# Kernel optimization log

Hardware: AMD Instinct MI355X
Metric: run time of the kernel (lower is better)

Reference implementation:

```python
import jax, jax.numpy as jnp
import numpy as np
from math import ceil

B, T, FEAT, F1, ACTION_DIM, ATOMS = 128, 128, 256, 512, 6, 32


def _make_masks(f1, action_dim, atoms):
    # Faithful numpy replication of ActorMultiEnv_v2.create_weigth_mask
    sz = action_dim * atoms
    aux1, aux2 = sz, f1
    dvs = [0]
    w = np.zeros([f1, sz], np.float32)
    we = np.zeros([f1, f1], np.float32)
    for i in range(sz):
        dv = aux2 / aux1
        v = ceil(dv) if dv - int(dv) > 0.5 else int(dv)
        s = int(np.sum(dvs))
        w[s:s + v, i] = 1.0 / v
        we[s:s + v, s:s + v] = 1.0
        dvs.append(v)
        aux1 -= 1
        aux2 -= v
    sizes = np.array([3, 5, 7, 9, 11, 15, 19, 25, 35])
    m = int(sizes[np.argmin(np.abs(max(dvs[1:]) - sizes))])
    return w, we, m, int(ceil(f1 / m))


def setup_inputs() -> dict:
    key = jax.random.key(0)
    ks = jax.random.split(key, 16)

    def he(k, shape):
        return jax.random.normal(k, shape, jnp.float32) * np.float32(np.sqrt(2.0 / shape[0]))

    w_np, we_np, m, sz_mini = _make_masks(F1, ACTION_DIM, ATOMS)
    return {
        "features": jax.random.normal(ks[0], (B, T, FEAT), jnp.float32),
        "W_hat1": he(ks[1], (FEAT, F1)),
        "M_hat1": he(ks[2], (FEAT, F1)),
        "G1": he(ks[3], (FEAT, F1)),
        "W_hat2": he(ks[4], (F1, F1)),
        "M_hat2": he(ks[5], (F1, F1)),
        "G2": he(ks[6], (F1, F1)),
        "W1e": he(ks[7], (2 * F1, F1)),
        "b1e": jnp.zeros((F1,), jnp.float32),
        "W2e": he(ks[8], (F1, F1)),
        "b2e": jnp.zeros((F1,), jnp.float32),
        "W3": he(ks[9], (F1, F1)),
        "b3": jnp.zeros((F1,), jnp.float32),
        "kn": he(ks[10], (m, m)),
        "w": jnp.asarray(w_np),
        "we": jnp.asarray(we_np),
        "sz_mini": sz_mini,
        "action_dim": ACTION_DIM,
        "atoms": ATOMS,
    }


def _nalu_pair(x1, x2, W_hat, M_hat, G):
    # NALU transform with two stacked output branches (additive, gated-nalu)
    W = jnp.tanh(W_hat) * jax.nn.sigmoid(M_hat)
    a = x1 @ W
    m = jnp.exp(jnp.clip(jnp.log(jnp.abs(x2) + 1e-7) @ W, -20.0, 20.0))
    g = jax.nn.sigmoid(x1 @ G)
    return jax.nn.gelu(a), jax.nn.gelu(g * a + (1.0 - g) * m)


def reference(features, W_hat1, M_hat1, G1, W_hat2, M_hat2, G2,
              W1e, b1e, W2e, b2e, W3, b3, kn, w, we,
              sz_mini, action_dim, atoms):
    # fc1 / fc2 (nalu_transform): two stacked branches on axis 1
    h11, h12 = _nalu_pair(features, features, W_hat1, M_hat1, G1)   # [B,T,f1] each
    ha, ht = _nalu_pair(h11, h12, W_hat2, M_hat2, G2)
    h = jnp.concatenate([ha, ht], axis=-1)                           # [B,T,2*f1]

    f1 = we.shape[0]
    # block-diagonal tiling of the per-env mini-kernel, masked by 'we'
    Keff = jnp.kron(jnp.eye(sz_mini, dtype=kn.dtype), kn)[:f1, :f1] * we  # [f1,f1]

    xa1 = jax.nn.gelu((h @ W1e + b1e) @ Keff)    # fc1e: dense -> block-masked mini-kernel matmul
    xa2 = jax.nn.gelu((xa1 @ W2e + b2e) @ Keff)  # fc2e
    v = xa2 @ (W3 * we) + b3                     # fc3: masked dense
    o = (xa1 @ w).reshape(xa1.shape[0], xa1.shape[1], action_dim, atoms)
    return o, v
```

## Files before the change

### kernel.cpp

```cpp
#include <hip/hip_runtime.h>
#include <hip/hip_bf16.h>
#include <hip/hip_fp16.h>

#define NROWS 16384
#define FEATD 256
#define F1D   512
#define SZD   192

typedef unsigned short u16;
typedef float    f32x4  __attribute__((ext_vector_type(4)));
typedef short    bf16x8 __attribute__((ext_vector_type(8)));
typedef _Float16 f16x8  __attribute__((ext_vector_type(8)));
typedef unsigned short u16x8 __attribute__((ext_vector_type(8)));

#define LO_SCALE 2048.0f
#define LO_INV   (1.0f / 2048.0f)

__device__ __forceinline__ float sigmoid_f(float x) { return 1.0f / (1.0f + expf(-x)); }

__device__ __forceinline__ float gelu_f(float x) {
    float x3 = x * x * x;
    float inner = 0.7978845608028654f * (x + 0.044715f * x3);
    return 0.5f * x * (1.0f + tanhf(inner));
}

__device__ __forceinline__ u16 f2bf(float f) {
    unsigned u = __float_as_uint(f);
    u = (u + 0x7FFFu + ((u >> 16) & 1u)) >> 16;
    return (u16)u;
}
__device__ __forceinline__ float bf2f(u16 h) { return __uint_as_float(((unsigned)h) << 16); }

__device__ __forceinline__ void split8(float4 a, float4 b, u16x8& hi, u16x8& lo) {
    float v[8] = {a.x, a.y, a.z, a.w, b.x, b.y, b.z, b.w};
    #pragma unroll
    for (int i = 0; i < 8; ++i) {
        u16 h = f2bf(v[i]);
        hi[i] = h;
        lo[i] = f2bf(v[i] - bf2f(h));
    }
}

__device__ __forceinline__ u16 f2h_u(float f)  { return __half_as_ushort(__float2half(f)); }
__device__ __forceinline__ float h2f_u(u16 u)  { return __half2float(__ushort_as_half(u)); }

__device__ __forceinline__ void split8hs(float4 a, float4 b, u16x8& hi, u16x8& lo) {
    float v[8] = {a.x, a.y, a.z, a.w, b.x, b.y, b.z, b.w};
    #pragma unroll
    for (int i = 0; i < 8; ++i) {
        u16 h = f2h_u(v[i]);
        hi[i] = h;
        lo[i] = f2h_u((v[i] - h2f_u(h)) * LO_SCALE);
    }
}

__device__ __forceinline__ int lofs(int row, int chunk) {
    return row * 32 + ((chunk ^ ((row >> 1) & 3)) << 3);
}

__global__ void wprep_f16_kernel(const float* __restrict__ src, const float* __restrict__ src2,
                                 u16* __restrict__ dhi, u16* __restrict__ dlo, int Kd, int Nd)
{
    int idx = blockIdx.x * blockDim.x + threadIdx.x;
    if (idx >= Kd * Nd) return;
    int n = idx / Kd, k = idx - n * Kd;
    float v = src[(size_t)k * Nd + n];
    if (src2) v = tanhf(v) * sigmoid_f(src2[(size_t)k * Nd + n]);
    u16 h = f2h_u(v);
    dhi[idx] = h;
    dlo[idx] = f2h_u((v - h2f_u(h)) * LO_SCALE);
}

__global__ void wprep2_kernel(const float* __restrict__ src,
                              u16* __restrict__ dhi, u16* __restrict__ dlo, int Kd, int Nd)
{
    int idx = blockIdx.x * blockDim.x + threadIdx.x;
    if (idx >= Kd * Nd) return;
    int n = idx / Kd, k = idx - n * Kd;
    float v = src[(size_t)k * Nd + n];
    u16 h = f2bf(v);
    dhi[idx] = h;
    dlo[idx] = f2bf(v - bf2f(h));
}

__global__ __launch_bounds__(512)
void prep2_kernel(const float* __restrict__ kn, const float* __restrict__ we,
                  const float* __restrict__ W3,
                  float* __restrict__ Kb, float* __restrict__ W3b, int m)
{
    int j = threadIdx.x;
    if (j >= F1D) return;
    int jb = (j / m) * m;
    int jm = j - jb;
    for (int t = 0; t < 4; ++t) {
        int i = jb + t;
        float v = 0.0f;
        if (t < m && i < F1D)
            v = kn[t * m + jm] * we[(size_t)i * F1D + j];
        Kb[t * F1D + j] = v;
    }
    for (int d = 0; d < 15; ++d) {
        int i = j - 7 + d;
        float v = 0.0f;
        if (i >= 0 && i < F1D)
            v = W3[(size_t)i * F1D + j] * we[(size_t)i * F1D + j];
        W3b[d * F1D + j] = v;
    }
}

__global__ void colrange_wband_kernel(const float* __restrict__ w, int* __restrict__ cs,
                                      float* __restrict__ wb)
{
    int c = blockIdx.x * blockDim.x + threadIdx.x;
    if (c >= SZD) return;
    int s = 0, e = -1;
    for (int r = 0; r < F1D; ++r) {
        if (w[(size_t)r * SZD + c] != 0.0f) { if (e < 0) s = r; e = r; }
    }
    cs[c] = s;
    for (int t = 0; t < 4; ++t)
        wb[t * SZD + c] = (s + t <= e) ? w[(size_t)(s + t) * SZD + c] : 0.0f;
}

template<int K, bool LOGX2, bool WRITE_LOG>
__global__ __launch_bounds__(256)
void nalu_mfma_kernel(const float* __restrict__ x1, const float* __restrict__ x2,
                      const u16* __restrict__ Wh, const u16* __restrict__ Wl,
                      const u16* __restrict__ Gh, const u16* __restrict__ Gl,
                      float* __restrict__ out1, float* __restrict__ out2, int ld_out)
{
    __shared__ u16 A1h[64 * 32], A1l[64 * 32];
    __shared__ u16 A2h[64 * 32], A2l[64 * 32];
    __shared__ u16 BWh[64 * 32], BWl[64 * 32];
    __shared__ u16 BGh[64 * 32], BGl[64 * 32];

    const int t = threadIdx.x;
    const int lane = t & 63;
    const int wv = t >> 6;
    const int wr = wv >> 1, wc = wv & 1;
    const int lr = lane & 15, lk = lane >> 4;
    const int row0 = blockIdx.y * 64;
    const int col0 = blockIdx.x * 64;
    const int sr = t >> 2;
    const int kc = t & 3;

    f32x4 aA[2][2], aAx[2][2], aM[2][2], aMx[2][2], aG[2][2], aGx[2][2];
    #pragma unroll
    for (int i = 0; i < 2; ++i)
        #pragma unroll
        for (int j = 0; j < 2; ++j) {
            aA[i][j] = 0; aAx[i][j] = 0;
            aM[i][j] = 0; aMx[i][j] = 0;
            aG[i][j] = 0; aGx[i][j] = 0;
        }

    for (int k0 = 0; k0 < K; k0 += 32) {
        const float* px1 = x1 + (size_t)(row0 + sr) * K + k0 + kc * 8;
        float4 f0 = *(const float4*)px1;
        float4 f1 = *(const float4*)(px1 + 4);
        u16x8 v1h, v1l;
        split8hs(f0, f1, v1h, v1l);
        float4 e0, e1;
        if (LOGX2) {
            e0.x = logf(fabsf(f0.x) + 1e-7f); e0.y = logf(fabsf(f0.y) + 1e-7f);
            e0.z = logf(fabsf(f0.z) + 1e-7f); e0.w = logf(fabsf(f0.w) + 1e-7f);
            e1.x = logf(fabsf(f1.x) + 1e-7f); e1.y = logf(fabsf(f1.y) + 1e-7f);
            e1.z = logf(fabsf(f1.z) + 1e-7f); e1.w = logf(fabsf(f1.w) + 1e-7f);
        } else {
            const float* px2 = x2 + (size_t)(row0 + sr) * K + k0 + kc * 8;
            e0 = *(const float4*)px2;
            e1 = *(const float4*)(px2 + 4);
        }
        u16x8 v2h, v2l;
        split8hs(e0, e1, v2h, v2l);
        u16x8 vwh = *(const u16x8*)(Wh + (size_t)(col0 + sr) * K + k0 + kc * 8);
        u16x8 vwl = *(const u16x8*)(Wl + (size_t)(col0 + sr) * K + k0 + kc * 8);
        u16x8 vgh = *(const u16x8*)(Gh + (size_t)(col0 + sr) * K + k0 + kc * 8);
        u16x8 vgl = *(const u16x8*)(Gl + (size_t)(col0 + sr) * K + k0 + kc * 8);

        __syncthreads();
        {
            int o = lofs(sr, kc);
            *(u16x8*)&A1h[o] = v1h;  *(u16x8*)&A1l[o] = v1l;
            *(u16x8*)&A2h[o] = v2h;  *(u16x8*)&A2l[o] = v2l;
            *(u16x8*)&BWh[o] = vwh;  *(u16x8*)&BWl[o] = vwl;
            *(u16x8*)&BGh[o] = vgh;  *(u16x8*)&BGl[o] = vgl;
        }
        __syncthreads();

        #pragma unroll
        for (int fc = 0; fc < 2; ++fc) {
            const int bo = lofs(wc * 32 + fc * 16 + lr, lk);
            f16x8 bwh = *(f16x8*)&BWh[bo];
            f16x8 bwl = *(f16x8*)&BWl[bo];
            f16x8 bgh = *(f16x8*)&BGh[bo];
            f16x8 bgl = *(f16x8*)&BGl[bo];
            #pragma unroll
            for (int fr = 0; fr < 2; ++fr) {
                const int ao = lofs(wr * 32 + fr * 16 + lr, lk);
                f16x8 a1h = *(f16x8*)&A1h[ao];
                f16x8 a1l = *(f16x8*)&A1l[ao];
                f16x8 a2h = *(f16x8*)&A2h[ao];
                f16x8 a2l = *(f16x8*)&A2l[ao];
                aA [fr][fc] = __builtin_amdgcn_mfma_f32_16x16x32_f16(a1h, bwh, aA [fr][fc], 0, 0, 0);
                aAx[fr][fc] = __builtin_amdgcn_mfma_f32_16x16x32_f16(a1h, bwl, aAx[fr][fc], 0, 0, 0);
                aAx[fr][fc] = __builtin_amdgcn_mfma_f32_16x16x32_f16(a1l, bwh, aAx[fr][fc], 0, 0, 0);
                aM [fr][fc] = __builtin_amdgcn_mfma_f32_16x16x32_f16(a2h, bwh, aM [fr][fc], 0, 0, 0);
                aMx[fr][fc] = __builtin_amdgcn_mfma_f32_16x16x32_f16(a2h, bwl, aMx[fr][fc], 0, 0, 0);
                aMx[fr][fc] = __builtin_amdgcn_mfma_f32_16x16x32_f16(a2l, bwh, aMx[fr][fc], 0, 0, 0);
                aG [fr][fc] = __builtin_amdgcn_mfma_f32_16x16x32_f16(a1h, bgh, aG [fr][fc], 0, 0, 0);
                aGx[fr][fc] = __builtin_amdgcn_mfma_f32_16x16x32_f16(a1h, bgl, aGx[fr][fc], 0, 0, 0);
                aGx[fr][fc] = __builtin_amdgcn_mfma_f32_16x16x32_f16(a1l, bgh, aGx[fr][fc], 0, 0, 0);
            }
        }
    }

    #pragma unroll
    for (int fr = 0; fr < 2; ++fr)
        #pragma unroll
        for (int fc = 0; fc < 2; ++fc) {
            int colg = col0 + wc * 32 + fc * 16 + lr;
            int rowb = row0 + wr * 32 + fr * 16 + lk * 4;
            #pragma unroll
            for (int i = 0; i < 4; ++i) {
                float a  = aA[fr][fc][i] + aAx[fr][fc][i] * LO_INV;
                float mm = aM[fr][fc][i] + aMx[fr][fc][i] * LO_INV;
                float g  = aG[fr][fc][i] + aGx[fr][fc][i] * LO_INV;
                float m_ = expf(fminf(fmaxf(mm, -20.0f), 20.0f));
                float gs = sigmoid_f(g);
                float h11v = gelu_f(a);
                float h12v = gelu_f(gs * a + (1.0f - gs) * m_);
                out1[(size_t)(rowb + i) * ld_out + colg] = h11v;
                out2[(size_t)(rowb + i) * ld_out + colg] =
                    WRITE_LOG ? logf(fabsf(h12v) + 1e-7f) : h12v;
            }
        }
}

template<int K>
__global__ __launch_bounds__(256)
void gemm_mfma_kernel(const float* __restrict__ A,
                      const u16* __restrict__ Bh, const u16* __restrict__ Bl,
                      const float* __restrict__ bias, float* __restrict__ out)
{
    __shared__ u16 Ah[128 * 32], Al[128 * 32];
    __shared__ u16 Bsh[64 * 32], Bsl[64 * 32];

    const int t = threadIdx.x;
    const int lane = t & 63;
    const int wv = t >> 6;
    const int wr = wv >> 1, wc = wv & 1;
    const int lr = lane & 15, lk = lane >> 4;
    const int row0 = blockIdx.y * 128;
    const int col0 = blockIdx.x * 64;
    const int sr = t >> 2;
    const int kc = t & 3;

    f32x4 acc[4][2];
    #pragma unroll
    for (int i = 0; i < 4; ++i)
        #pragma unroll
        for (int j = 0; j < 2; ++j) acc[i][j] = 0;

    for (int k0 = 0; k0 < K; k0 += 32) {
        u16x8 vah[2], val[2];
        #pragma unroll
        for (int p = 0; p < 2; ++p) {
            int r = p * 64 + sr;
            const float* pa = A + (size_t)(row0 + r) * K + k0 + kc * 8;
            float4 f0 = *(const float4*)pa;
            float4 f1 = *(const float4*)(pa + 4);
            split8(f0, f1, vah[p], val[p]);
        }
        u16x8 vbh = *(const u16x8*)(Bh + (size_t)(col0 + sr) * K + k0 + kc * 8);
        u16x8 vbl = *(const u16x8*)(Bl + (size_t)(col0 + sr) * K + k0 + kc * 8);

        __syncthreads();
        #pragma unroll
        for (int p = 0; p < 2; ++p) {
            int o = lofs(p * 64 + sr, kc);
            *(u16x8*)&Ah[o] = vah[p];
            *(u16x8*)&Al[o] = val[p];
        }
        {
            int o = lofs(sr, kc);
            *(u16x8*)&Bsh[o] = vbh;
            *(u16x8*)&Bsl[o] = vbl;
        }
        __syncthreads();

        #pragma unroll
        for (int fc = 0; fc < 2; ++fc) {
            const int bo = lofs(wc * 32 + fc * 16 + lr, lk);
            bf16x8 bh = *(bf16x8*)&Bsh[bo];
            bf16x8 bl = *(bf16x8*)&Bsl[bo];
            #pragma unroll
            for (int fr = 0; fr < 4; ++fr) {
                const int ao = lofs(wr * 64 + fr * 16 + lr, lk);
                bf16x8 ah = *(bf16x8*)&Ah[ao];
                bf16x8 al = *(bf16x8*)&Al[ao];
                f32x4 a = acc[fr][fc];
                a = __builtin_amdgcn_mfma_f32_16x16x32_bf16(ah, bh, a, 0, 0, 0);
                a = __builtin_amdgcn_mfma_f32_16x16x32_bf16(ah, bl, a, 0, 0, 0);
                a = __builtin_amdgcn_mfma_f32_16x16x32_bf16(al, bh, a, 0, 0, 0);
                acc[fr][fc] = a;
            }
        }
    }

    #pragma unroll
    for (int fr = 0; fr < 4; ++fr)
        #pragma unroll
        for (int fc = 0; fc < 2; ++fc) {
            int colg = col0 + wc * 32 + fc * 16 + lr;
            int rowb = row0 + wr * 64 + fr * 16 + lk * 4;
            float bv = bias[colg];
            #pragma unroll
            for (int i = 0; i < 4; ++i)
                out[(size_t)(rowb + i) * F1D + colg] = acc[fr][fc][i] + bv;
        }
}

template<int ROWS>
__global__ __launch_bounds__(256)
void kxo_kernel(const float* __restrict__ pre1, const float* __restrict__ Kb,
                const float* __restrict__ wb, const int* __restrict__ cs,
                float* __restrict__ xa1, float* __restrict__ o_out, int m)
{
    __shared__ float sKb[4][F1D];
    __shared__ float swb[4][SZD];
    __shared__ int   scs[SZD];
    __shared__ float spre[2][F1D];
    __shared__ float sxa[2][F1D];

    const int t = threadIdx.x;
    for (int i = t; i < 4 * F1D; i += 256) sKb[i >> 9][i & 511] = Kb[i];
    for (int i = t; i < 4 * SZD; i += 256) swb[i / SZD][i % SZD] = wb[i];
    if (t < SZD) scs[t] = cs[t];

    const int row_base = blockIdx.x * ROWS;
    const int rr = t >> 7;
    const int jc = t & 127;

    for (int ch = 0; ch < ROWS; ch += 2) {
        const int r0 = row_base + ch;
        __syncthreads();
        ((float4*)&spre[0][0])[t] = *(const float4*)(pre1 + (size_t)r0 * F1D + t * 4);
        __syncthreads();

        #pragma unroll
        for (int kk = 0; kk < 4; ++kk) {
            int j  = jc + (kk << 7);
            int jb = (j / m) * m;
            float s = 0.0f;
            for (int tt = 0; tt < 4; ++tt) {
                int i2 = jb + tt; if (i2 > F1D - 1) i2 = F1D - 1;
                s = fmaf(spre[rr][i2], sKb[tt][j], s);
            }
            float g = gelu_f(s);
            sxa[rr][j] = g;
            xa1[(size_t)(r0 + rr) * F1D + j] = g;
        }
        __syncthreads();

        for (int pos = t; pos < 2 * SZD; pos += 256) {
            int rr2 = pos / SZD, c = pos - rr2 * SZD;
            int s0 = scs[c];
            float s = 0.0f;
            #pragma unroll
            for (int tt = 0; tt < 4; ++tt) {
                int i2 = s0 + tt; if (i2 > F1D - 1) i2 = F1D - 1;
                s = fmaf(sxa[rr2][i2], swb[tt][c], s);
            }
            o_out[(size_t)(r0 + rr2) * SZD + c] = s;
        }
    }
}

template<int ROWS>
__global__ __launch_bounds__(256)
void kv_kernel(const float* __restrict__ pre2, const float* __restrict__ Kb,
               const float* __restrict__ W3b, const float* __restrict__ b3,
               float* __restrict__ v_out, int m)
{
    __shared__ float sW3[15][F1D];
    __shared__ float sKb[4][F1D];
    __shared__ float sb3[F1D];
    __shared__ float spre[2][F1D];
    __shared__ float sxa[2][F1D];

    const int t = threadIdx.x;
    for (int i = t; i < 15 * F1D; i += 256) sW3[i >> 9][i & 511] = W3b[i];
    for (int i = t; i < 4 * F1D; i += 256)  sKb[i >> 9][i & 511] = Kb[i];
    for (int i = t; i < F1D; i += 256)      sb3[i] = b3[i];

    const int row_base = blockIdx.x * ROWS;
    const int rr = t >> 7;
    const int jc = t & 127;

    for (int ch = 0; ch < ROWS; ch += 2) {
        const int r0 = row_base + ch;
        __syncthreads();
        ((float4*)&spre[0][0])[t] = *(const float4*)(pre2 + (size_t)r0 * F1D + t * 4);
        __syncthreads();

        #pragma unroll
        for (int kk = 0; kk < 4; ++kk) {
            int j  = jc + (kk << 7);
            int jb = (j / m) * m;
            float s = 0.0f;
            for (int tt = 0; tt < 4; ++tt) {
                int i2 = jb + tt; if (i2 > F1D - 1) i2 = F1D - 1;
                s = fmaf(spre[rr][i2], sKb[tt][j], s);
            }
            sxa[rr][j] = gelu_f(s);
        }
        __syncthreads();

        #pragma unroll
        for (int kk = 0; kk < 4; ++kk) {
            int j = jc + (kk << 7);
            float s = sb3[j];
            #pragma unroll
            for (int d = 0; d < 15; ++d) {
                int i2 = j - 7 + d;
                if (i2 < 0) i2 = 0; if (i2 > F1D - 1) i2 = F1D - 1;
                s = fmaf(sxa[rr][i2], sW3[d][j], s);
            }
            v_out[(size_t)(r0 + rr) * F1D + j] = s;
        }
    }
}

extern "C" void kernel_launch(void* const* d_in, const int* in_sizes, int n_in,
                              void* d_out, int out_size, void* d_ws, size_t ws_size,
                              hipStream_t stream)
{
    const float* features = (const float*)d_in[0];
    const float* Wh1 = (const float*)d_in[1];
    const float* Mh1 = (const float*)d_in[2];
    const float* G1  = (const float*)d_in[3];
    const float* Wh2 = (const float*)d_in[4];
    const float* Mh2 = (const float*)d_in[5];
    const float* G2  = (const float*)d_in[6];
    const float* W1e = (const float*)d_in[7];
    const float* b1e = (const float*)d_in[8];
    const float* W2e = (const float*)d_in[9];
    const float* b2e = (const float*)d_in[10];
    const float* W3  = (const float*)d_in[11];
    const float* b3  = (const float*)d_in[12];
    const float* kn  = (const float*)d_in[13];
    const float* w   = (const float*)d_in[14];
    const float* we  = (const float*)d_in[15];

    int m = 1;
    { int s = in_sizes[13]; while (m * m < s) ++m; }

    char* base = (char*)d_ws;
    size_t off = 0;
    auto alloc = [&](size_t bytes) { void* p = base + off; off += (bytes + 255) & ~255ull; return p; };
    u16*   W1h  = (u16*)alloc((size_t)F1D * FEATD * 2);
    u16*   W1l  = (u16*)alloc((size_t)F1D * FEATD * 2);
    u16*   G1h  = (u16*)alloc((size_t)F1D * FEATD * 2);
    u16*   G1l  = (u16*)alloc((size_t)F1D * FEATD * 2);
    u16*   W2h  = (u16*)alloc((size_t)F1D * F1D * 2);
    u16*   W2l  = (u16*)alloc((size_t)F1D * F1D * 2);
    u16*   G2h  = (u16*)alloc((size_t)F1D * F1D * 2);
    u16*   G2l  = (u16*)alloc((size_t)F1D * F1D * 2);
    u16*   W1eh = (u16*)alloc((size_t)F1D * 2 * F1D * 2);
    u16*   W1el = (u16*)alloc((size_t)F1D * 2 * F1D * 2);
    u16*   W2eh = (u16*)alloc((size_t)F1D * F1D * 2);
    u16*   W2el = (u16*)alloc((size_t)F1D * F1D * 2);
    float* Kb   = (float*)alloc(4 * F1D * 4);
    float* W3b  = (float*)alloc(15 * F1D * 4);
    float* wb   = (float*)alloc(4 * SZD * 4);
    int*   cs   = (int*)alloc(SZD * 4);
    float* h11  = (float*)alloc((size_t)NROWS * F1D * 4);
    float* lh12 = (float*)alloc((size_t)NROWS * F1D * 4);
    float* hb   = (float*)alloc((size_t)NROWS * 2 * F1D * 4);

    float* o_out = (float*)d_out;
    float* v_out = (float*)d_out + (size_t)NROWS * SZD;
    float* xa1   = v_out;

    wprep_f16_kernel<<<(F1D * FEATD + 255) / 256, 256, 0, stream>>>(Wh1, Mh1, W1h, W1l, FEATD, F1D);
    wprep_f16_kernel<<<(F1D * FEATD + 255) / 256, 256, 0, stream>>>(G1, nullptr, G1h, G1l, FEATD, F1D);
    wprep_f16_kernel<<<(F1D * F1D + 255) / 256, 256, 0, stream>>>(Wh2, Mh2, W2h, W2l, F1D, F1D);
    wprep_f16_kernel<<<(F1D * F1D + 255) / 256, 256, 0, stream>>>(G2, nullptr, G2h, G2l, F1D, F1D);
    wprep2_kernel<<<(F1D * 2 * F1D + 255) / 256, 256, 0, stream>>>(W1e, W1eh, W1el, 2 * F1D, F1D);
    wprep2_kernel<<<(F1D * F1D + 255) / 256, 256, 0, stream>>>(W2e, W2eh, W2el, F1D, F1D);
    prep2_kernel<<<1, 512, 0, stream>>>(kn, we, W3, Kb, W3b, m);
    colrange_wband_kernel<<<1, 256, 0, stream>>>(w, cs, wb);

    dim3 gN(F1D / 64, NROWS / 64);
    dim3 gG(F1D / 64, NROWS / 128);

    nalu_mfma_kernel<FEATD, true, true><<<gN, 256, 0, stream>>>(
        features, features, W1h, W1l, G1h, G1l, h11, lh12, F1D);
    nalu_mfma_kernel<F1D, false, false><<<gN, 256, 0, stream>>>(
        h11, lh12, W2h, W2l, G2h, G2l, hb, hb + F1D, 2 * F1D);

    float* pre1 = h11;
    gemm_mfma_kernel<2 * F1D><<<gG, 256, 0, stream>>>(hb, W1eh, W1el, b1e, pre1);

    kxo_kernel<8><<<NROWS / 8, 256, 0, stream>>>(pre1, Kb, wb, cs, xa1, o_out, m);

    float* pre2 = lh12;
    gemm_mfma_kernel<F1D><<<gG, 256, 0, stream>>>(xa1, W2eh, W2el, b2e, pre2);

    kv_kernel<8><<<NROWS / 8, 256, 0, stream>>>(pre2, Kb, W3b, b3, v_out, m);
}
```

Before: 568.1 us.

## Store intermediates as pre-split hi/lo half pairs and swizzle tiles across XCDs

```diff
diff --git a/kernel.cpp b/kernel.cpp
--- a/kernel.cpp
+++ b/kernel.cpp
@@ -30,16 +30,6 @@
     return (u16)u;
 }
 __device__ __forceinline__ float bf2f(u16 h) { return __uint_as_float(((unsigned)h) << 16); }
-
-__device__ __forceinline__ void split8(float4 a, float4 b, u16x8& hi, u16x8& lo) {
-    float v[8] = {a.x, a.y, a.z, a.w, b.x, b.y, b.z, b.w};
-    #pragma unroll
-    for (int i = 0; i < 8; ++i) {
-        u16 h = f2bf(v[i]);
-        hi[i] = h;
-        lo[i] = f2bf(v[i] - bf2f(h));
-    }
-}
 
 __device__ __forceinline__ u16 f2h_u(float f)  { return __half_as_ushort(__float2half(f)); }
 __device__ __forceinline__ float h2f_u(u16 u)  { return __half2float(__ushort_as_half(u)); }
@@ -56,6 +46,15 @@
 
 __device__ __forceinline__ int lofs(int row, int chunk) {
     return row * 32 + ((chunk ^ ((row >> 1) & 3)) << 3);
+}
+
+__device__ __forceinline__ void xcd_tile(int TM, int& row0, int& col0) {
+    int b   = blockIdx.x + gridDim.x * blockIdx.y;
+    int nwg = gridDim.x * gridDim.y;
+    int q   = nwg >> 3;
+    int swz = (b & 7) * q + (b >> 3);
+    col0 = (swz & 7) * 64;
+    row0 = (swz >> 3) * TM;
 }
 
 __global__ void wprep_f16_kernel(const float* __restrict__ src, const float* __restrict__ src2,
@@ -122,12 +121,13 @@
         wb[t * SZD + c] = (s + t <= e) ? w[(size_t)(s + t) * SZD + c] : 0.0f;
 }
 
-template<int K, bool LOGX2, bool WRITE_LOG>
+template<int K>
 __global__ __launch_bounds__(256)
-void nalu_mfma_kernel(const float* __restrict__ x1, const float* __restrict__ x2,
-                      const u16* __restrict__ Wh, const u16* __restrict__ Wl,
-                      const u16* __restrict__ Gh, const u16* __restrict__ Gl,
-                      float* __restrict__ out1, float* __restrict__ out2, int ld_out)
+void nalu_l1_kernel(const float* __restrict__ x1,
+                    const u16* __restrict__ Wh, const u16* __restrict__ Wl,
+                    const u16* __restrict__ Gh, const u16* __restrict__ Gl,
+                    u16* __restrict__ o1h, u16* __restrict__ o1l,
+                    u16* __restrict__ o2h, u16* __restrict__ o2l)
 {
     __shared__ u16 A1h[64 * 32], A1l[64 * 32];
     __shared__ u16 A2h[64 * 32], A2l[64 * 32];
@@ -139,8 +139,8 @@
     const int wv = t >> 6;
     const int wr = wv >> 1, wc = wv & 1;
     const int lr = lane & 15, lk = lane >> 4;
-    const int row0 = blockIdx.y * 64;
-    const int col0 = blockIdx.x * 64;
+    int row0, col0;
+    xcd_tile(64, row0, col0);
     const int sr = t >> 2;
     const int kc = t & 3;
 
@@ -161,16 +161,10 @@
         u16x8 v1h, v1l;
         split8hs(f0, f1, v1h, v1l);
         float4 e0, e1;
-        if (LOGX2) {
-            e0.x = logf(fabsf(f0.x) + 1e-7f); e0.y = logf(fabsf(f0.y) + 1e-7f);
-            e0.z = logf(fabsf(f0.z) + 1e-7f); e0.w = logf(fabsf(f0.w) + 1e-7f);
-            e1.x = logf(fabsf(f1.x) + 1e-7f); e1.y = logf(fabsf(f1.y) + 1e-7f);
-            e1.z = logf(fabsf(f1.z) + 1e-7f); e1.w = logf(fabsf(f1.w) + 1e-7f);
-        } else {
-            const float* px2 = x2 + (size_t)(row0 + sr) * K + k0 + kc * 8;
-            e0 = *(const float4*)px2;
-            e1 = *(const float4*)(px2 + 4);
-        }
+        e0.x = logf(fabsf(f0.x) + 1e-7f); e0.y = logf(fabsf(f0.y) + 1e-7f);
+        e0.z = logf(fabsf(f0.z) + 1e-7f); e0.w = logf(fabsf(f0.w) + 1e-7f);
+        e1.x = logf(fabsf(f1.x) + 1e-7f); e1.y = logf(fabsf(f1.y) + 1e-7f);
+        e1.z = logf(fabsf(f1.z) + 1e-7f); e1.w = logf(fabsf(f1.w) + 1e-7f);
         u16x8 v2h, v2l;
         split8hs(e0, e1, v2h, v2l);
         u16x8 vwh = *(const u16x8*)(Wh + (size_t)(col0 + sr) * K + k0 + kc * 8);
@@ -230,29 +224,142 @@
                 float gs = sigmoid_f(g);
                 float h11v = gelu_f(a);
                 float h12v = gelu_f(gs * a + (1.0f - gs) * m_);
-                out1[(size_t)(rowb + i) * ld_out + colg] = h11v;
-                out2[(size_t)(rowb + i) * ld_out + colg] =
-                    WRITE_LOG ? logf(fabsf(h12v) + 1e-7f) : h12v;
+                float lgv  = logf(fabsf(h12v) + 1e-7f);
+                size_t oi = (size_t)(rowb + i) * F1D + colg;
+                u16 hh = f2h_u(h11v);
+                o1h[oi] = hh;
+                o1l[oi] = f2h_u((h11v - h2f_u(hh)) * LO_SCALE);
+                u16 lh = f2h_u(lgv);
+                o2h[oi] = lh;
+                o2l[oi] = f2h_u((lgv - h2f_u(lh)) * LO_SCALE);
             }
         }
 }
 
 template<int K>
 __global__ __launch_bounds__(256)
-void gemm_mfma_kernel(const float* __restrict__ A,
-                      const u16* __restrict__ Bh, const u16* __restrict__ Bl,
-                      const float* __restrict__ bias, float* __restrict__ out)
-{
-    __shared__ u16 Ah[128 * 32], Al[128 * 32];
-    __shared__ u16 Bsh[64 * 32], Bsl[64 * 32];
+void nalu_l2_kernel(const u16* __restrict__ x1h, const u16* __restrict__ x1l,
+                    const u16* __restrict__ x2h, const u16* __restrict__ x2l,
+                    const u16* __restrict__ Wh, const u16* __restrict__ Wl,
+                    const u16* __restrict__ Gh, const u16* __restrict__ Gl,
+                    u16* __restrict__ ohh, u16* __restrict__ ohl)
+{
+    __shared__ u16 A1h[64 * 32], A1l[64 * 32];
+    __shared__ u16 A2h[64 * 32], A2l[64 * 32];
+    __shared__ u16 BWh[64 * 32], BWl[64 * 32];
+    __shared__ u16 BGh[64 * 32], BGl[64 * 32];
 
     const int t = threadIdx.x;
     const int lane = t & 63;
     const int wv = t >> 6;
     const int wr = wv >> 1, wc = wv & 1;
     const int lr = lane & 15, lk = lane >> 4;
-    const int row0 = blockIdx.y * 128;
-    const int col0 = blockIdx.x * 64;
+    int row0, col0;
+    xcd_tile(64, row0, col0);
+    const int sr = t >> 2;
+    const int kc = t & 3;
+
+    f32x4 aA[2][2], aAx[2][2], aM[2][2], aMx[2][2], aG[2][2], aGx[2][2];
+    #pragma unroll
+    for (int i = 0; i < 2; ++i)
+        #pragma unroll
+        for (int j = 0; j < 2; ++j) {
+            aA[i][j] = 0; aAx[i][j] = 0;
+            aM[i][j] = 0; aMx[i][j] = 0;
+            aG[i][j] = 0; aGx[i][j] = 0;
+        }
+
+    for (int k0 = 0; k0 < K; k0 += 32) {
+        const size_t arow = (size_t)(row0 + sr) * K + k0 + kc * 8;
+        const size_t brow = (size_t)(col0 + sr) * K + k0 + kc * 8;
+        u16x8 v1h = *(const u16x8*)(x1h + arow);
+        u16x8 v1l = *(const u16x8*)(x1l + arow);
+        u16x8 v2h = *(const u16x8*)(x2h + arow);
+        u16x8 v2l = *(const u16x8*)(x2l + arow);
+        u16x8 vwh = *(const u16x8*)(Wh + brow);
+        u16x8 vwl = *(const u16x8*)(Wl + brow);
+        u16x8 vgh = *(const u16x8*)(Gh + brow);
+        u16x8 vgl = *(const u16x8*)(Gl + brow);
+
+        __syncthreads();
+        {
+            int o = lofs(sr, kc);
+            *(u16x8*)&A1h[o] = v1h;  *(u16x8*)&A1l[o] = v1l;
+            *(u16x8*)&A2h[o] = v2h;  *(u16x8*)&A2l[o] = v2l;
+            *(u16x8*)&BWh[o] = vwh;  *(u16x8*)&BWl[o] = vwl;
+            *(u16x8*)&BGh[o] = vgh;  *(u16x8*)&BGl[o] = vgl;
+        }
+        __syncthreads();
+
+        #pragma unroll
+        for (int fc = 0; fc < 2; ++fc) {
+            const int bo = lofs(wc * 32 + fc * 16 + lr, lk);
+            f16x8 bwh = *(f16x8*)&BWh[bo];
+            f16x8 bwl = *(f16x8*)&BWl[bo];
+            f16x8 bgh = *(f16x8*)&BGh[bo];
+            f16x8 bgl = *(f16x8*)&BGl[bo];
+            #pragma unroll
+            for (int fr = 0; fr < 2; ++fr) {
+                const int ao = lofs(wr * 32 + fr * 16 + lr, lk);
+                f16x8 a1h = *(f16x8*)&A1h[ao];
+                f16x8 a1l = *(f16x8*)&A1l[ao];
+                f16x8 a2h = *(f16x8*)&A2h[ao];
+                f16x8 a2l = *(f16x8*)&A2l[ao];
+                aA [fr][fc] = __builtin_amdgcn_mfma_f32_16x16x32_f16(a1h, bwh, aA [fr][fc], 0, 0, 0);
+                aAx[fr][fc] = __builtin_amdgcn_mfma_f32_16x16x32_f16(a1h, bwl, aAx[fr][fc], 0, 0, 0);
+                aAx[fr][fc] = __builtin_amdgcn_mfma_f32_16x16x32_f16(a1l, bwh, aAx[fr][fc], 0, 0, 0);
+                aM [fr][fc] = __builtin_amdgcn_mfma_f32_16x16x32_f16(a2h, bwh, aM [fr][fc], 0, 0, 0);
+                aMx[fr][fc] = __builtin_amdgcn_mfma_f32_16x16x32_f16(a2h, bwl, aMx[fr][fc], 0, 0, 0);
+                aMx[fr][fc] = __builtin_amdgcn_mfma_f32_16x16x32_f16(a2l, bwh, aMx[fr][fc], 0, 0, 0);
+                aG [fr][fc] = __builtin_amdgcn_mfma_f32_16x16x32_f16(a1h, bgh, aG [fr][fc], 0, 0, 0);
+                aGx[fr][fc] = __builtin_amdgcn_mfma_f32_16x16x32_f16(a1h, bgl, aGx[fr][fc], 0, 0, 0);
+                aGx[fr][fc] = __builtin_amdgcn_mfma_f32_16x16x32_f16(a1l, bgh, aGx[fr][fc], 0, 0, 0);
+            }
+        }
+    }
+
+    #pragma unroll
+    for (int fr = 0; fr < 2; ++fr)
+        #pragma unroll
+        for (int fc = 0; fc < 2; ++fc) {
+            int colg = col0 + wc * 32 + fc * 16 + lr;
+            int rowb = row0 + wr * 32 + fr * 16 + lk * 4;
+            #pragma unroll
+            for (int i = 0; i < 4; ++i) {
+                float a  = aA[fr][fc][i] + aAx[fr][fc][i] * LO_INV;
+                float mm = aM[fr][fc][i] + aMx[fr][fc][i] * LO_INV;
+                float g  = aG[fr][fc][i] + aGx[fr][fc][i] * LO_INV;
+                float m_ = expf(fminf(fmaxf(mm, -20.0f), 20.0f));
+                float gs = sigmoid_f(g);
+                float hav = gelu_f(a);
+                float htv = gelu_f(gs * a + (1.0f - gs) * m_);
+                size_t base = (size_t)(rowb + i) * (2 * F1D) + colg;
+                u16 ah = f2bf(hav);
+                ohh[base] = ah;
+                ohl[base] = f2bf(hav - bf2f(ah));
+                u16 th = f2bf(htv);
+                ohh[base + F1D] = th;
+                ohl[base + F1D] = f2bf(htv - bf2f(th));
+            }
+        }
+}
+
+template<int K>
+__global__ __launch_bounds__(256)
+void gemm_mfma_kernel(const u16* __restrict__ Ahp, const u16* __restrict__ Alp,
+                      const u16* __restrict__ Bh, const u16* __restrict__ Bl,
+                      const float* __restrict__ bias, float* __restrict__ out)
+{
+    __shared__ u16 Ah[128 * 32], Al[128 * 32];
+    __shared__ u16 Bsh[64 * 32], Bsl[64 * 32];
+
+    const int t = threadIdx.x;
+    const int lane = t & 63;
+    const int wv = t >> 6;
+    const int wr = wv >> 1, wc = wv & 1;
+    const int lr = lane & 15, lk = lane >> 4;
+    int row0, col0;
+    xcd_tile(128, row0, col0);
     const int sr = t >> 2;
     const int kc = t & 3;
 
@@ -266,14 +373,13 @@
         u16x8 vah[2], val[2];
         #pragma unroll
         for (int p = 0; p < 2; ++p) {
-            int r = p * 64 + sr;
-            const float* pa = A + (size_t)(row0 + r) * K + k0 + kc * 8;
-            float4 f0 = *(const float4*)pa;
-            float4 f1 = *(const float4*)(pa + 4);
-            split8(f0, f1, vah[p], val[p]);
-        }
-        u16x8 vbh = *(const u16x8*)(Bh + (size_t)(col0 + sr) * K + k0 + kc * 8);
-        u16x8 vbl = *(const u16x8*)(Bl + (size_t)(col0 + sr) * K + k0 + kc * 8);
+            const size_t arow = (size_t)(row0 + p * 64 + sr) * K + k0 + kc * 8;
+            vah[p] = *(const u16x8*)(Ahp + arow);
+            val[p] = *(const u16x8*)(Alp + arow);
+        }
+        const size_t brow = (size_t)(col0 + sr) * K + k0 + kc * 8;
+        u16x8 vbh = *(const u16x8*)(Bh + brow);
+        u16x8 vbl = *(const u16x8*)(Bl + brow);
 
         __syncthreads();
         #pragma unroll
@@ -325,7 +431,8 @@
 __global__ __launch_bounds__(256)
 void kxo_kernel(const float* __restrict__ pre1, const float* __restrict__ Kb,
                 const float* __restrict__ wb, const int* __restrict__ cs,
-                float* __restrict__ xa1, float* __restrict__ o_out, int m)
+                u16* __restrict__ xa1h, u16* __restrict__ xa1l,
+                float* __restrict__ o_out, int m)
 {
     __shared__ float sKb[4][F1D];
     __shared__ float swb[4][SZD];
@@ -359,7 +466,10 @@
             }
             float g = gelu_f(s);
             sxa[rr][j] = g;
-            xa1[(size_t)(r0 + rr) * F1D + j] = g;
+            size_t oi = (size_t)(r0 + rr) * F1D + j;
+            u16 gh = f2bf(g);
+            xa1h[oi] = gh;
+            xa1l[oi] = f2bf(g - bf2f(gh));
         }
         __syncthreads();
 
@@ -475,13 +585,19 @@
     float* W3b  = (float*)alloc(15 * F1D * 4);
     float* wb   = (float*)alloc(4 * SZD * 4);
     int*   cs   = (int*)alloc(SZD * 4);
-    float* h11  = (float*)alloc((size_t)NROWS * F1D * 4);
-    float* lh12 = (float*)alloc((size_t)NROWS * F1D * 4);
-    float* hb   = (float*)alloc((size_t)NROWS * 2 * F1D * 4);
+    u16*   h11h = (u16*)alloc((size_t)NROWS * F1D * 2);
+    u16*   h11l = (u16*)alloc((size_t)NROWS * F1D * 2);
+    u16*   l12h = (u16*)alloc((size_t)NROWS * F1D * 2);
+    u16*   l12l = (u16*)alloc((size_t)NROWS * F1D * 2);
+    u16*   hbh  = (u16*)alloc((size_t)NROWS * 2 * F1D * 2);
+    u16*   hbl  = (u16*)alloc((size_t)NROWS * 2 * F1D * 2);
+    float* pre1 = (float*)h11h;
+    float* pre2 = (float*)l12h;
 
     float* o_out = (float*)d_out;
     float* v_out = (float*)d_out + (size_t)NROWS * SZD;
-    float* xa1   = v_out;
+    u16* xa1h = (u16*)v_out;
+    u16* xa1l = xa1h + (size_t)NROWS * F1D;
 
     wprep_f16_kernel<<<(F1D * FEATD + 255) / 256, 256, 0, stream>>>(Wh1, Mh1, W1h, W1l, FEATD, F1D);
     wprep_f16_kernel<<<(F1D * FEATD + 255) / 256, 256, 0, stream>>>(G1, nullptr, G1h, G1l, FEATD, F1D);
@@ -495,18 +611,16 @@
     dim3 gN(F1D / 64, NROWS / 64);
     dim3 gG(F1D / 64, NROWS / 128);
 
-    nalu_mfma_kernel<FEATD, true, true><<<gN, 256, 0, stream>>>(
-        features, features, W1h, W1l, G1h, G1l, h11, lh12, F1D);
-    nalu_mfma_kernel<F1D, false, false><<<gN, 256, 0, stream>>>(
-        h11, lh12, W2h, W2l, G2h, G2l, hb, hb + F1D, 2 * F1D);
-
-    float* pre1 = h11;
-    gemm_mfma_kernel<2 * F1D><<<gG, 256, 0, stream>>>(hb, W1eh, W1el, b1e, pre1);
-
-    kxo_kernel<8><<<NROWS / 8, 256, 0, stream>>>(pre1, Kb, wb, cs, xa1, o_out, m);
-
-    float* pre2 = lh12;
-    gemm_mfma_kernel<F1D><<<gG, 256, 0, stream>>>(xa1, W2eh, W2el, b2e, pre2);
+    nalu_l1_kernel<FEATD><<<gN, 256, 0, stream>>>(
+        features, W1h, W1l, G1h, G1l, h11h, h11l, l12h, l12l);
+    nalu_l2_kernel<F1D><<<gN, 256, 0, stream>>>(
+        h11h, h11l, l12h, l12l, W2h, W2l, G2h, G2l, hbh, hbl);
+
+    gemm_mfma_kernel<2 * F1D><<<gG, 256, 0, stream>>>(hbh, hbl, W1eh, W1el, b1e, pre1);
+
+    kxo_kernel<8><<<NROWS / 8, 256, 0, stream>>>(pre1, Kb, wb, cs, xa1h, xa1l, o_out, m);
+
+    gemm_mfma_kernel<F1D><<<gG, 256, 0, stream>>>(xa1h, xa1l, W2eh, W2el, b2e, pre2);
 
     kv_kernel<8><<<NROWS / 8, 256, 0, stream>>>(pre2, Kb, W3b, b3, v_out, m);
 }
```

Measured after the change: 536.7 us. 1.06x faster.
